# Optimization experiments

Hardware: AMD Instinct MI355X
Metric: run time of the kernel (lower is better)

The kernel has to match this reference:

```python
import jax, jax.numpy as jnp
import numpy as np

B, S, E, H = 8, 512, 1024, 16
Dh = E // H
MAX_LEN = 512


def setup_inputs() -> dict:
    key = jax.random.key(0)
    ks = jax.random.split(key, 16)
    std = 1.0 / np.sqrt(E)
    inp = {
        "query": jax.random.normal(ks[0], (B, S, E), jnp.float32),
        "key": jax.random.normal(ks[1], (B, S, E), jnp.float32),
        "value": jax.random.normal(ks[2], (B, S, E), jnp.float32),
        "Wq": jax.random.normal(ks[3], (E, E), jnp.float32) * std,
        "bq": jax.random.normal(ks[4], (E,), jnp.float32) * std,
        "Wk": jax.random.normal(ks[5], (E, E), jnp.float32) * std,
        "bk": jax.random.normal(ks[6], (E,), jnp.float32) * std,
        "Wv": jax.random.normal(ks[7], (E, E), jnp.float32) * std,
        "bv": jax.random.normal(ks[8], (E,), jnp.float32) * std,
        "Wo": jax.random.normal(ks[9], (E, E), jnp.float32) * std,
        "bo": jax.random.normal(ks[10], (E,), jnp.float32) * std,
        "pos": jax.random.normal(ks[11], (MAX_LEN, 1, E), jnp.float32),
    }
    return inp


def reference(query, key, value, Wq, bq, Wk, bk, Wv, bv, Wo, bo, pos):
    b, sq, e = query.shape
    s = min(sq, key.shape[1])  # target_seq_length (static)
    scale = np.sqrt(Dh).astype(np.float32)
    pe = pos[:s, 0, :][None]  # [1, s, E] broadcast over batch
    q = query[:, :s] @ Wq.T + bq + pe
    k = key[:, :s] @ Wk.T + bk + pe
    v = value[:, :s] @ Wv.T + bv + pe
    # [b, s, H, Dh]
    q = q.reshape(b, s, H, Dh)
    k = k.reshape(b, s, H, Dh)
    v = v.reshape(b, s, H, Dh)
    scores = jnp.einsum("bqhd,bkhd->bhqk", q, k) / scale
    attn = jax.nn.softmax(scores, axis=-1)
    wv = jnp.einsum("bhqk,bkhd->bqhd", attn, v).reshape(b, s, e)
    return wv @ Wo.T + bo
```

## Files before the change

### kernel.cpp

```cpp
#include <hip/hip_runtime.h>
#include <hip/hip_bf16.h>

typedef __attribute__((ext_vector_type(8))) short bfx8;
typedef __attribute__((ext_vector_type(4))) short bfx4;
typedef __attribute__((ext_vector_type(4))) float fx4;

static __device__ __forceinline__ short f2bf(float f) {
  union { float f; unsigned u; } v; v.f = f;
  unsigned r = v.u + 0x7fffu + ((v.u >> 16) & 1u);
  return (short)(r >> 16);
}

static __device__ __forceinline__ void gld16(const void* g, void* l) {
  __builtin_amdgcn_global_load_lds(
      (const __attribute__((address_space(1))) void*)g,
      (__attribute__((address_space(3))) void*)l, 16, 0, 0);
}

constexpr int Bz = 8, Sq = 512, Em = 1024, Hn = 16, Dh = 64;
constexpr int Mrows = Bz * Sq;
constexpr size_t NE = (size_t)Mrows * Em;
constexpr size_t WE = (size_t)Em * Em;

__global__ __launch_bounds__(256) void convert_kernel(
    const float* __restrict__ q, const float* __restrict__ k,
    const float* __restrict__ v,
    const float* __restrict__ Wq, const float* __restrict__ Wk,
    const float* __restrict__ Wv, const float* __restrict__ Wo,
    short* __restrict__ qx, short* __restrict__ kx, short* __restrict__ vx,
    short* __restrict__ wqb, short* __restrict__ wkb,
    short* __restrict__ wvb, short* __restrict__ wob)
{
  const size_t c = (size_t)blockIdx.x * 256 + threadIdx.x;
  constexpr size_t CI = NE / 8;
  constexpr size_t CW = WE / 8;
  const float* src; short* dst; size_t off;
  if (c < 3 * CI) {
    const int sgi = (int)(c / CI);
    src = sgi == 0 ? q : sgi == 1 ? k : v;
    dst = sgi == 0 ? qx : sgi == 1 ? kx : vx;
    off = (c - (size_t)sgi * CI) * 8;
  } else {
    const size_t w = c - 3 * CI;
    const int sgi = (int)(w / CW);
    src = sgi == 0 ? Wq : sgi == 1 ? Wk : sgi == 2 ? Wv : Wo;
    dst = sgi == 0 ? wqb : sgi == 1 ? wkb : sgi == 2 ? wvb : wob;
    off = (w - (size_t)sgi * CW) * 8;
  }
  fx4 a = *(const fx4*)(src + off);
  fx4 b = *(const fx4*)(src + off + 4);
  bfx8 o = { f2bf(a[0]), f2bf(a[1]), f2bf(a[2]), f2bf(a[3]),
             f2bf(b[0]), f2bf(b[1]), f2bf(b[2]), f2bf(b[3]) };
  *(bfx8*)(dst + off) = o;
}

__global__ __launch_bounds__(512, 2) void gemm_qkv_bf16(
    const short* __restrict__ qx, const short* __restrict__ kx,
    const short* __restrict__ vx,
    const short* __restrict__ Wqb, const short* __restrict__ Wkb,
    const short* __restrict__ Wvb,
    const float* __restrict__ bq, const float* __restrict__ bk,
    const float* __restrict__ bv,
    const float* __restrict__ pos,
    short* __restrict__ qb, short* __restrict__ kb, short* __restrict__ vb)
{
  __shared__ short SM[65536];

  const int z = blockIdx.z;
  const short* X = (z == 0) ? qx : (z == 1) ? kx : vx;
  const short* W = (z == 0) ? Wqb : (z == 1) ? Wkb : Wvb;
  const float* bias = (z == 0) ? bq : (z == 1) ? bk : bv;
  short* dst = (z == 0) ? qb : (z == 1) ? kb : vb;

  const int t0b = blockIdx.x * 256;
  const int f0 = blockIdx.y * 256;
  const int t = threadIdx.x, lane = t & 63, wave = t >> 6;
  const int wr = wave >> 2;
  const int wn = wave & 3;
  const int fr = lane & 15, fq = lane >> 4;

  const int srow = t >> 2;
  const int scol = ((t & 3) ^ ((t >> 3) & 3)) * 8;
  const short* gA = W + (size_t)(f0 + srow) * Em + scol;
  const short* gB = X + (size_t)(t0b + srow) * Em + scol;
  const int ldst = wave * 512;

  auto stage = [&](int ktn) {
    short* sl = SM + (ktn & 3) * 16384;
    const int ko = ktn * 32;
#pragma unroll
    for (int g = 0; g < 2; ++g) {
      gld16(gA + (size_t)(g * 128) * Em + ko, sl + g * 4096 + ldst);
      gld16(gB + (size_t)(g * 128) * Em + ko, sl + 8192 + g * 4096 + ldst);
    }
  };

  const int csw = (fq ^ ((fr >> 1) & 3)) * 8;

  fx4 acc[8][4] = {};

  stage(0); stage(1); stage(2);
  for (int kt = 0; kt < 32; ++kt) {
    if (kt < 29) stage(kt + 3);
    __builtin_amdgcn_sched_barrier(0);
    if (kt < 29)       asm volatile("s_waitcnt vmcnt(12)");
    else if (kt == 29) asm volatile("s_waitcnt vmcnt(8)");
    else if (kt == 30) asm volatile("s_waitcnt vmcnt(4)");
    else               asm volatile("s_waitcnt vmcnt(0)");
    __builtin_amdgcn_sched_barrier(0);
    __builtin_amdgcn_s_barrier();

    const short* slA = SM + (kt & 3) * 16384;
    const short* slB = slA + 8192;

    bfx8 af[8], bf[4];
#pragma unroll
    for (int rg = 0; rg < 8; ++rg)
      af[rg] = *(const bfx8*)&slA[(wr * 128 + rg * 16 + fr) * 32 + csw];
#pragma unroll
    for (int cg = 0; cg < 4; ++cg)
      bf[cg] = *(const bfx8*)&slB[(wn * 64 + cg * 16 + fr) * 32 + csw];

    __builtin_amdgcn_s_setprio(1);
#pragma unroll
    for (int rg = 0; rg < 8; ++rg)
#pragma unroll
      for (int cg = 0; cg < 4; ++cg)
        acc[rg][cg] = __builtin_amdgcn_mfma_f32_16x16x32_bf16(
            af[rg], bf[cg], acc[rg][cg], 0, 0, 0);
    __builtin_amdgcn_s_setprio(0);
    __builtin_amdgcn_sched_barrier(0);
    __builtin_amdgcn_s_barrier();
  }

  const int b = t0b >> 9;
  if (z < 2) {
#pragma unroll
    for (int fp = 0; fp < 2; ++fp) {
      if (fp) __syncthreads();
      if (wr == fp) {
#pragma unroll
        for (int rg = 0; rg < 8; ++rg) {
          const int nloc = rg * 16 + fq * 4;
          const int nng = f0 + fp * 128 + nloc;
          const fx4 bb = *(const fx4*)&bias[nng];
#pragma unroll
          for (int cg = 0; cg < 4; ++cg) {
            const int token = wn * 64 + cg * 16 + fr;
            const int s = (t0b + token) & (Sq - 1);
            const fx4 pe = *(const fx4*)&pos[(size_t)s * Em + nng];
            const fx4 a = acc[rg][cg];
            bfx4 o = { f2bf(a[0] + bb[0] + pe[0]), f2bf(a[1] + bb[1] + pe[1]),
                       f2bf(a[2] + bb[2] + pe[2]), f2bf(a[3] + bb[3] + pe[3]) };
            *(bfx4*)&SM[token * 136 + nloc] = o;
          }
        }
      }
      __syncthreads();
#pragma unroll
      for (int it = 0; it < 8; ++it) {
        const int flat = it * 512 + t;
        const int token = flat >> 4, ch = flat & 15;
        bfx8 val = *(const bfx8*)&SM[token * 136 + ch * 8];
        const int nng = f0 + fp * 128 + ch * 8;
        const int h = nng >> 6, d = nng & 63;
        const int s = (t0b + token) & (Sq - 1);
        *(bfx8*)&dst[(((size_t)b * Hn + h) * Sq + s) * Dh + d] = val;
      }
    }
  } else {
#pragma unroll
    for (int fp = 0; fp < 2; ++fp) {
      if (fp) __syncthreads();
      if (wr == fp) {
#pragma unroll
        for (int rg = 0; rg < 8; ++rg) {
          const int nloc = rg * 16 + fq * 4;
          const int nng = f0 + fp * 128 + nloc;
          const fx4 bb = *(const fx4*)&bias[nng];
#pragma unroll
          for (int cg = 0; cg < 4; ++cg) {
            const int token = wn * 64 + cg * 16 + fr;
            const int s = (t0b + token) & (Sq - 1);
            const fx4 pe = *(const fx4*)&pos[(size_t)s * Em + nng];
            const fx4 a = acc[rg][cg];
#pragma unroll
            for (int i = 0; i < 4; ++i)
              SM[(nloc + i) * 264 + token] = f2bf(a[i] + bb[i] + pe[i]);
          }
        }
      }
      __syncthreads();
      const int s0 = t0b & (Sq - 1);
#pragma unroll
      for (int it = 0; it < 8; ++it) {
        const int flat = it * 512 + t;
        const int row = flat >> 5, ch = flat & 31;
        bfx8 val = *(const bfx8*)&SM[row * 264 + ch * 8];
        const int nng = f0 + fp * 128 + row;
        const int h = nng >> 6, d = nng & 63;
        *(bfx8*)&dst[(((size_t)b * Hn + h) * Dh + d) * Sq + s0 + ch * 8] = val;
      }
    }
  }
}

constexpr int LDP = 136;

__global__ __launch_bounds__(256, 4) void gemm_out_bf16(
    const short* __restrict__ wv, const short* __restrict__ Wob,
    const float* __restrict__ bo, float* __restrict__ out)
{
  __shared__ short SMo[2 * 8192];
  short* As = SMo;
  short* Bs = SMo + 8192;

  const int m0 = blockIdx.x * 128;
  const int n0 = blockIdx.y * 128;
  const int t = threadIdx.x, lane = t & 63, wave = t >> 6;
  const int wr = wave >> 1, wc = wave & 1;
  const int fr = lane & 15, fq = lane >> 4;

  const int trow = t >> 3;
  const int scol = ((t & 7) ^ (trow & 7)) * 8;
  const short* gW = Wob + (size_t)(n0 + trow) * Em + scol;
  const short* gX = wv + (size_t)(m0 + trow) * Em + scol;
  short* lA = As + wave * 512;
  short* lB = Bs + wave * 512;

  const int sw0 = ((fq ^ (fr & 7)) * 8);
  const int sw1 = (((4 + fq) ^ (fr & 7)) * 8);

  fx4 acc[4][4] = {};

  for (int k0 = 0; k0 < Em; k0 += 64) {
#pragma unroll
    for (int r = 0; r < 4; ++r) {
      gld16(gW + (size_t)(32 * r) * Em + k0, lA + r * 2048);
      gld16(gX + (size_t)(32 * r) * Em + k0, lB + r * 2048);
    }
    __syncthreads();

#pragma unroll
    for (int ks = 0; ks < 2; ++ks) {
      const int sw = ks ? sw1 : sw0;
      bfx8 af[4], bf[4];
#pragma unroll
      for (int u = 0; u < 4; ++u)
        af[u] = *(const bfx8*)&As[(wr * 64 + u * 16 + fr) * 64 + sw];
#pragma unroll
      for (int v = 0; v < 4; ++v)
        bf[v] = *(const bfx8*)&Bs[(wc * 64 + v * 16 + fr) * 64 + sw];
#pragma unroll
      for (int u = 0; u < 4; ++u)
#pragma unroll
        for (int v = 0; v < 4; ++v)
          acc[u][v] = __builtin_amdgcn_mfma_f32_16x16x32_bf16(af[u], bf[v], acc[u][v], 0, 0, 0);
    }
    __syncthreads();
  }

#pragma unroll
  for (int u = 0; u < 4; ++u) {
    const int nn = n0 + wr * 64 + u * 16 + fq * 4;
    const fx4 bb = *(const fx4*)&bo[nn];
#pragma unroll
    for (int v = 0; v < 4; ++v) {
      const int m = m0 + wc * 64 + v * 16 + fr;
      fx4 val = acc[u][v];
      val[0] += bb[0]; val[1] += bb[1]; val[2] += bb[2]; val[3] += bb[3];
      *(fx4*)&out[(size_t)m * Em + nn] = val;
    }
  }
}

constexpr int KVB = 64, LDK = 72;

__global__ __launch_bounds__(512) void attn_kernel(
    const short* __restrict__ qb, const short* __restrict__ kb,
    const short* __restrict__ vb, short* __restrict__ wv)
{
  __shared__ short Ks[KVB * LDK];
  __shared__ short Vt[Dh * LDK];
  __shared__ short Ps[8][16 * LDK];

  const int bh = blockIdx.x;
  const int qt = blockIdx.y;
  const int t = threadIdx.x, lane = t & 63, wave = t >> 6;
  const int fr = lane & 15, fq = lane >> 4;

  const size_t base = (size_t)bh * Sq * Dh;
  const int q0 = qt * 128 + wave * 16;

  bfx8 qf[2];
  {
    const short* qp = qb + base + (size_t)(q0 + fr) * Dh;
    qf[0] = *(const bfx8*)(qp + fq * 8);
    qf[1] = *(const bfx8*)(qp + 32 + fq * 8);
  }

  const int kr = t >> 3, kc = (t & 7) * 8;
  const short* kbp = kb + base + (size_t)kr * Dh + kc;
  const short* vbp = vb + base + (size_t)kr * Sq + kc;

  {
    bfx8 k0 = *(const bfx8*)kbp;
    bfx8 v0 = *(const bfx8*)vbp;
    *(bfx8*)&Ks[kr * LDK + kc] = k0;
    *(bfx8*)&Vt[kr * LDK + kc] = v0;
  }
  __syncthreads();

  float mrow[4] = { -1e30f, -1e30f, -1e30f, -1e30f };
  float lrow[4] = { 0.f, 0.f, 0.f, 0.f };
  fx4 oacc[4] = {};

  for (int kv0 = 0; kv0 < Sq; kv0 += KVB) {
    const bool more = (kv0 + KVB) < Sq;
    bfx8 nk0, nv0;
    if (more) {
      nk0 = *(const bfx8*)(kbp + (size_t)(kv0 + KVB) * Dh);
      nv0 = *(const bfx8*)(vbp + kv0 + KVB);
    }

    fx4 sa[4] = {};
    __builtin_amdgcn_s_setprio(1);
#pragma unroll
    for (int nf = 0; nf < 4; ++nf) {
#pragma unroll
      for (int ks = 0; ks < 2; ++ks) {
        bfx8 kf = *(const bfx8*)&Ks[(nf * 16 + fr) * LDK + ks * 32 + fq * 8];
        sa[nf] = __builtin_amdgcn_mfma_f32_16x16x32_bf16(qf[ks], kf, sa[nf], 0, 0, 0);
      }
    }
    __builtin_amdgcn_s_setprio(0);

#pragma unroll
    for (int i = 0; i < 4; ++i) {
      float mx = fmaxf(fmaxf(sa[0][i], sa[1][i]), fmaxf(sa[2][i], sa[3][i]));
      mx = fmaxf(mx, __shfl_xor(mx, 1));
      mx = fmaxf(mx, __shfl_xor(mx, 2));
      mx = fmaxf(mx, __shfl_xor(mx, 4));
      mx = fmaxf(mx, __shfl_xor(mx, 8));
      mx *= 0.125f;
      if (mx > mrow[i] + 8.f) {
        const float alpha = __expf(mrow[i] - mx);
        mrow[i] = mx;
        lrow[i] *= alpha;
#pragma unroll
        for (int df = 0; df < 4; ++df) oacc[df][i] *= alpha;
      }
      float rs = 0.f;
#pragma unroll
      for (int nf = 0; nf < 4; ++nf) {
        const float p = __expf(sa[nf][i] * 0.125f - mrow[i]);
        rs += p;
        Ps[wave][(fq * 4 + i) * LDK + nf * 16 + fr] = f2bf(p);
      }
      rs += __shfl_xor(rs, 1);
      rs += __shfl_xor(rs, 2);
      rs += __shfl_xor(rs, 4);
      rs += __shfl_xor(rs, 8);
      lrow[i] += rs;
    }

    bfx8 pf[2];
    pf[0] = *(const bfx8*)&Ps[wave][fr * LDK + fq * 8];
    pf[1] = *(const bfx8*)&Ps[wave][fr * LDK + 32 + fq * 8];
    __builtin_amdgcn_s_setprio(1);
#pragma unroll
    for (int df = 0; df < 4; ++df) {
#pragma unroll
      for (int ks = 0; ks < 2; ++ks) {
        bfx8 vf = *(const bfx8*)&Vt[(df * 16 + fr) * LDK + ks * 32 + fq * 8];
        oacc[df] = __builtin_amdgcn_mfma_f32_16x16x32_bf16(pf[ks], vf, oacc[df], 0, 0, 0);
      }
    }
    __builtin_amdgcn_s_setprio(0);
    __syncthreads();

    if (more) {
      *(bfx8*)&Ks[kr * LDK + kc] = nk0;
      *(bfx8*)&Vt[kr * LDK + kc] = nv0;
      __syncthreads();
    }
  }

  const int b = bh >> 4, h = bh & 15;
#pragma unroll
  for (int df = 0; df < 4; ++df) {
    const int d = df * 16 + fr;
#pragma unroll
    for (int i = 0; i < 4; ++i) {
      const int qrow = q0 + fq * 4 + i;
      const float o = oacc[df][i] / lrow[i];
      wv[((size_t)b * Sq + qrow) * Em + h * Dh + d] = f2bf(o);
    }
  }
}

extern "C" void kernel_launch(void* const* d_in, const int* in_sizes, int n_in,
                              void* d_out, int out_size, void* d_ws, size_t ws_size,
                              hipStream_t stream) {
  (void)in_sizes; (void)n_in; (void)out_size; (void)ws_size;
  const float* query = (const float*)d_in[0];
  const float* key   = (const float*)d_in[1];
  const float* value = (const float*)d_in[2];
  const float* Wq = (const float*)d_in[3];
  const float* bq = (const float*)d_in[4];
  const float* Wk = (const float*)d_in[5];
  const float* bk = (const float*)d_in[6];
  const float* Wv = (const float*)d_in[7];
  const float* bv = (const float*)d_in[8];
  const float* Wo = (const float*)d_in[9];
  const float* bo = (const float*)d_in[10];
  const float* pos = (const float*)d_in[11];

  short* qx = (short*)d_ws;
  short* kx = qx + NE;
  short* vx = kx + NE;
  short* Wqb = vx + NE;
  short* Wkb = Wqb + WE;
  short* Wvb = Wkb + WE;
  short* Wob = Wvb + WE;
  short* qb = Wob + WE;
  short* wv = qx;
  short* kb = (short*)d_out;
  short* vb = kb + NE;

  convert_kernel<<<dim3(8192), 256, 0, stream>>>(
      query, key, value, Wq, Wk, Wv, Wo, qx, kx, vx, Wqb, Wkb, Wvb, Wob);
  gemm_qkv_bf16<<<dim3(Mrows / 256, Em / 256, 3), 512, 0, stream>>>(
      qx, kx, vx, Wqb, Wkb, Wvb, bq, bk, bv, pos, qb, kb, vb);
  attn_kernel<<<dim3(Bz * Hn, Sq / 128), 512, 0, stream>>>(qb, kb, vb, wv);
  gemm_out_bf16<<<dim3(Mrows / 128, Em / 128), 256, 0, stream>>>(
      wv, Wob, bo, (float*)d_out);
}
```

Measured before the change: 111.8 us.

## Shrink GEMM tiles and switch QKV projection to double-buffered pipeline

The QKV projection GEMM goes from a 256x256 tile with a 4-stage LDS ring to a 128x256 tile with 2-stage double buffering. Its LDS use drops to 48 KB and the occupancy hint rises to 4 blocks, and the epilogue is rewritten with an XOR swizzle on the transposed V store. The output projection GEMM tile also shrinks from 128x128 to 128x64, doubling its grid. The aim is more blocks and better latency hiding across the 256 CUs, at the cost of less data reuse per tile and a shallower prefetch pipeline.

```diff
diff --git a/kernel.cpp b/kernel.cpp
--- a/kernel.cpp
+++ b/kernel.cpp
@@ -54,7 +54,7 @@
   *(bfx8*)(dst + off) = o;
 }
 
-__global__ __launch_bounds__(512, 2) void gemm_qkv_bf16(
+__global__ __launch_bounds__(512, 4) void gemm_qkv_bf16(
     const short* __restrict__ qx, const short* __restrict__ kx,
     const short* __restrict__ vx,
     const short* __restrict__ Wqb, const short* __restrict__ Wkb,
@@ -64,7 +64,7 @@
     const float* __restrict__ pos,
     short* __restrict__ qb, short* __restrict__ kb, short* __restrict__ vb)
 {
-  __shared__ short SM[65536];
+  __shared__ short SM[24576];
 
   const int z = blockIdx.z;
   const short* X = (z == 0) ? qx : (z == 1) ? kx : vx;
@@ -73,10 +73,10 @@
   short* dst = (z == 0) ? qb : (z == 1) ? kb : vb;
 
   const int t0b = blockIdx.x * 256;
-  const int f0 = blockIdx.y * 256;
+  const int f0 = blockIdx.y * 128;
   const int t = threadIdx.x, lane = t & 63, wave = t >> 6;
-  const int wr = wave >> 2;
-  const int wn = wave & 3;
+  const int wf = wave & 1;
+  const int wt = wave >> 1;
   const int fr = lane & 15, fq = lane >> 4;
 
   const int srow = t >> 2;
@@ -85,137 +85,137 @@
   const short* gB = X + (size_t)(t0b + srow) * Em + scol;
   const int ldst = wave * 512;
 
-  auto stage = [&](int ktn) {
-    short* sl = SM + (ktn & 3) * 16384;
+  auto stage = [&](int ktn, int s) {
+    short* base = SM + s * 12288;
     const int ko = ktn * 32;
-#pragma unroll
-    for (int g = 0; g < 2; ++g) {
-      gld16(gA + (size_t)(g * 128) * Em + ko, sl + g * 4096 + ldst);
-      gld16(gB + (size_t)(g * 128) * Em + ko, sl + 8192 + g * 4096 + ldst);
-    }
+    gld16(gA + ko, base + ldst);
+    gld16(gB + ko, base + 4096 + ldst);
+    gld16(gB + (size_t)128 * Em + ko, base + 8192 + ldst);
   };
 
   const int csw = (fq ^ ((fr >> 1) & 3)) * 8;
 
-  fx4 acc[8][4] = {};
-
-  stage(0); stage(1); stage(2);
+  fx4 acc[4][4] = {};
+
+  stage(0, 0);
+  __builtin_amdgcn_sched_barrier(0);
+  asm volatile("s_waitcnt vmcnt(0)");
+  __builtin_amdgcn_sched_barrier(0);
+  __builtin_amdgcn_s_barrier();
+
   for (int kt = 0; kt < 32; ++kt) {
-    if (kt < 29) stage(kt + 3);
+    const int s = kt & 1;
+    const short* bA = SM + s * 12288;
+    const short* bB = bA + 4096;
+    const bool pre = (kt + 1 < 32);
+    if (pre) stage(kt + 1, s ^ 1);
     __builtin_amdgcn_sched_barrier(0);
-    if (kt < 29)       asm volatile("s_waitcnt vmcnt(12)");
-    else if (kt == 29) asm volatile("s_waitcnt vmcnt(8)");
-    else if (kt == 30) asm volatile("s_waitcnt vmcnt(4)");
-    else               asm volatile("s_waitcnt vmcnt(0)");
+
+    bfx8 af[4], bf[4];
+#pragma unroll
+    for (int u = 0; u < 4; ++u)
+      af[u] = *(const bfx8*)&bA[(wf * 64 + u * 16 + fr) * 32 + csw];
+#pragma unroll
+    for (int v = 0; v < 4; ++v)
+      bf[v] = *(const bfx8*)&bB[(wt * 64 + v * 16 + fr) * 32 + csw];
+
+    __builtin_amdgcn_s_setprio(1);
+#pragma unroll
+    for (int u = 0; u < 4; ++u)
+#pragma unroll
+      for (int v = 0; v < 4; ++v)
+        acc[u][v] = __builtin_amdgcn_mfma_f32_16x16x32_bf16(af[u], bf[v], acc[u][v], 0, 0, 0);
+    __builtin_amdgcn_s_setprio(0);
+    __builtin_amdgcn_sched_barrier(0);
+
+    if (pre) asm volatile("s_waitcnt vmcnt(0)");
     __builtin_amdgcn_sched_barrier(0);
     __builtin_amdgcn_s_barrier();
-
-    const short* slA = SM + (kt & 3) * 16384;
-    const short* slB = slA + 8192;
-
-    bfx8 af[8], bf[4];
-#pragma unroll
-    for (int rg = 0; rg < 8; ++rg)
-      af[rg] = *(const bfx8*)&slA[(wr * 128 + rg * 16 + fr) * 32 + csw];
-#pragma unroll
-    for (int cg = 0; cg < 4; ++cg)
-      bf[cg] = *(const bfx8*)&slB[(wn * 64 + cg * 16 + fr) * 32 + csw];
-
-    __builtin_amdgcn_s_setprio(1);
-#pragma unroll
-    for (int rg = 0; rg < 8; ++rg)
-#pragma unroll
-      for (int cg = 0; cg < 4; ++cg)
-        acc[rg][cg] = __builtin_amdgcn_mfma_f32_16x16x32_bf16(
-            af[rg], bf[cg], acc[rg][cg], 0, 0, 0);
-    __builtin_amdgcn_s_setprio(0);
-    __builtin_amdgcn_sched_barrier(0);
-    __builtin_amdgcn_s_barrier();
   }
 
   const int b = t0b >> 9;
   if (z < 2) {
 #pragma unroll
+    for (int p = 0; p < 2; ++p) {
+      if (p) __syncthreads();
+      if ((wt >> 1) == p) {
+#pragma unroll
+        for (int u = 0; u < 4; ++u) {
+          const int nloc = wf * 64 + u * 16 + fq * 4;
+          const int nng = f0 + nloc;
+          const fx4 bb = *(const fx4*)&bias[nng];
+#pragma unroll
+          for (int v = 0; v < 4; ++v) {
+            const int token = wt * 64 + v * 16 + fr;
+            const int tl = token - p * 128;
+            const int s = (t0b + token) & (Sq - 1);
+            const fx4 pe = *(const fx4*)&pos[(size_t)s * Em + nng];
+            const fx4 a = acc[u][v];
+            bfx4 o = { f2bf(a[0] + bb[0] + pe[0]), f2bf(a[1] + bb[1] + pe[1]),
+                       f2bf(a[2] + bb[2] + pe[2]), f2bf(a[3] + bb[3] + pe[3]) };
+            *(bfx4*)&SM[tl * 136 + nloc] = o;
+          }
+        }
+      }
+      __syncthreads();
+#pragma unroll
+      for (int it = 0; it < 4; ++it) {
+        const int flat = it * 512 + t;
+        const int tl = flat >> 4, ch = flat & 15;
+        bfx8 val = *(const bfx8*)&SM[tl * 136 + ch * 8];
+        const int nng = f0 + ch * 8;
+        const int h = nng >> 6, d = nng & 63;
+        const int s = (t0b + p * 128 + tl) & (Sq - 1);
+        *(bfx8*)&dst[(((size_t)b * Hn + h) * Sq + s) * Dh + d] = val;
+      }
+    }
+  } else {
+#pragma unroll
     for (int fp = 0; fp < 2; ++fp) {
       if (fp) __syncthreads();
-      if (wr == fp) {
-#pragma unroll
-        for (int rg = 0; rg < 8; ++rg) {
-          const int nloc = rg * 16 + fq * 4;
-          const int nng = f0 + fp * 128 + nloc;
+      if (wf == fp) {
+#pragma unroll
+        for (int u = 0; u < 4; ++u) {
+          const int nloc = u * 16 + fq * 4;
+          const int nng = f0 + fp * 64 + nloc;
           const fx4 bb = *(const fx4*)&bias[nng];
 #pragma unroll
-          for (int cg = 0; cg < 4; ++cg) {
-            const int token = wn * 64 + cg * 16 + fr;
+          for (int v = 0; v < 4; ++v) {
+            const int token = wt * 64 + v * 16 + fr;
             const int s = (t0b + token) & (Sq - 1);
             const fx4 pe = *(const fx4*)&pos[(size_t)s * Em + nng];
-            const fx4 a = acc[rg][cg];
-            bfx4 o = { f2bf(a[0] + bb[0] + pe[0]), f2bf(a[1] + bb[1] + pe[1]),
-                       f2bf(a[2] + bb[2] + pe[2]), f2bf(a[3] + bb[3] + pe[3]) };
-            *(bfx4*)&SM[token * 136 + nloc] = o;
+            const fx4 a = acc[u][v];
+#pragma unroll
+            for (int i = 0; i < 4; ++i) {
+              const int row = nloc + i;
+              SM[row * 264 + (token ^ ((row & 12) << 2))] = f2bf(a[i] + bb[i] + pe[i]);
+            }
           }
         }
       }
       __syncthreads();
-#pragma unroll
-      for (int it = 0; it < 8; ++it) {
-        const int flat = it * 512 + t;
-        const int token = flat >> 4, ch = flat & 15;
-        bfx8 val = *(const bfx8*)&SM[token * 136 + ch * 8];
-        const int nng = f0 + fp * 128 + ch * 8;
-        const int h = nng >> 6, d = nng & 63;
-        const int s = (t0b + token) & (Sq - 1);
-        *(bfx8*)&dst[(((size_t)b * Hn + h) * Sq + s) * Dh + d] = val;
-      }
-    }
-  } else {
-#pragma unroll
-    for (int fp = 0; fp < 2; ++fp) {
-      if (fp) __syncthreads();
-      if (wr == fp) {
-#pragma unroll
-        for (int rg = 0; rg < 8; ++rg) {
-          const int nloc = rg * 16 + fq * 4;
-          const int nng = f0 + fp * 128 + nloc;
-          const fx4 bb = *(const fx4*)&bias[nng];
-#pragma unroll
-          for (int cg = 0; cg < 4; ++cg) {
-            const int token = wn * 64 + cg * 16 + fr;
-            const int s = (t0b + token) & (Sq - 1);
-            const fx4 pe = *(const fx4*)&pos[(size_t)s * Em + nng];
-            const fx4 a = acc[rg][cg];
-#pragma unroll
-            for (int i = 0; i < 4; ++i)
-              SM[(nloc + i) * 264 + token] = f2bf(a[i] + bb[i] + pe[i]);
-          }
-        }
-      }
-      __syncthreads();
       const int s0 = t0b & (Sq - 1);
 #pragma unroll
-      for (int it = 0; it < 8; ++it) {
+      for (int it = 0; it < 4; ++it) {
         const int flat = it * 512 + t;
         const int row = flat >> 5, ch = flat & 31;
-        bfx8 val = *(const bfx8*)&SM[row * 264 + ch * 8];
-        const int nng = f0 + fp * 128 + row;
+        bfx8 val = *(const bfx8*)&SM[row * 264 + ((ch * 8) ^ ((row & 12) << 2))];
+        const int nng = f0 + fp * 64 + row;
         const int h = nng >> 6, d = nng & 63;
         *(bfx8*)&dst[(((size_t)b * Hn + h) * Dh + d) * Sq + s0 + ch * 8] = val;
       }
     }
   }
 }
-
-constexpr int LDP = 136;
 
 __global__ __launch_bounds__(256, 4) void gemm_out_bf16(
     const short* __restrict__ wv, const short* __restrict__ Wob,
     const float* __restrict__ bo, float* __restrict__ out)
 {
-  __shared__ short SMo[2 * 8192];
-  short* As = SMo;
-  short* Bs = SMo + 8192;
-
-  const int m0 = blockIdx.x * 128;
+  __shared__ short As[128 * 64];
+  __shared__ short Bs[64 * 64];
+
+  const int m0 = blockIdx.x * 64;
   const int n0 = blockIdx.y * 128;
   const int t = threadIdx.x, lane = t & 63, wave = t >> 6;
   const int wr = wave >> 1, wc = wave & 1;
@@ -225,36 +225,36 @@
   const int scol = ((t & 7) ^ (trow & 7)) * 8;
   const short* gW = Wob + (size_t)(n0 + trow) * Em + scol;
   const short* gX = wv + (size_t)(m0 + trow) * Em + scol;
-  short* lA = As + wave * 512;
-  short* lB = Bs + wave * 512;
+  const int lofs = wave * 512;
 
   const int sw0 = ((fq ^ (fr & 7)) * 8);
   const int sw1 = (((4 + fq) ^ (fr & 7)) * 8);
 
-  fx4 acc[4][4] = {};
+  fx4 acc[4][2] = {};
 
   for (int k0 = 0; k0 < Em; k0 += 64) {
 #pragma unroll
-    for (int r = 0; r < 4; ++r) {
-      gld16(gW + (size_t)(32 * r) * Em + k0, lA + r * 2048);
-      gld16(gX + (size_t)(32 * r) * Em + k0, lB + r * 2048);
-    }
+    for (int g = 0; g < 4; ++g)
+      gld16(gW + (size_t)(32 * g) * Em + k0, As + g * 2048 + lofs);
+#pragma unroll
+    for (int g = 0; g < 2; ++g)
+      gld16(gX + (size_t)(32 * g) * Em + k0, Bs + g * 2048 + lofs);
     __syncthreads();
 
 #pragma unroll
     for (int ks = 0; ks < 2; ++ks) {
       const int sw = ks ? sw1 : sw0;
-      bfx8 af[4], bf[4];
+      bfx8 af[4], bf[2];
 #pragma unroll
       for (int u = 0; u < 4; ++u)
         af[u] = *(const bfx8*)&As[(wr * 64 + u * 16 + fr) * 64 + sw];
 #pragma unroll
-      for (int v = 0; v < 4; ++v)
-        bf[v] = *(const bfx8*)&Bs[(wc * 64 + v * 16 + fr) * 64 + sw];
+      for (int v = 0; v < 2; ++v)
+        bf[v] = *(const bfx8*)&Bs[(wc * 32 + v * 16 + fr) * 64 + sw];
 #pragma unroll
       for (int u = 0; u < 4; ++u)
 #pragma unroll
-        for (int v = 0; v < 4; ++v)
+        for (int v = 0; v < 2; ++v)
           acc[u][v] = __builtin_amdgcn_mfma_f32_16x16x32_bf16(af[u], bf[v], acc[u][v], 0, 0, 0);
     }
     __syncthreads();
@@ -265,8 +265,8 @@
     const int nn = n0 + wr * 64 + u * 16 + fq * 4;
     const fx4 bb = *(const fx4*)&bo[nn];
 #pragma unroll
-    for (int v = 0; v < 4; ++v) {
-      const int m = m0 + wc * 64 + v * 16 + fr;
+    for (int v = 0; v < 2; ++v) {
+      const int m = m0 + wc * 32 + v * 16 + fr;
       fx4 val = acc[u][v];
       val[0] += bb[0]; val[1] += bb[1]; val[2] += bb[2]; val[3] += bb[3];
       *(fx4*)&out[(size_t)m * Em + nn] = val;
@@ -430,9 +430,9 @@
 
   convert_kernel<<<dim3(8192), 256, 0, stream>>>(
       query, key, value, Wq, Wk, Wv, Wo, qx, kx, vx, Wqb, Wkb, Wvb, Wob);
-  gemm_qkv_bf16<<<dim3(Mrows / 256, Em / 256, 3), 512, 0, stream>>>(
+  gemm_qkv_bf16<<<dim3(Mrows / 256, Em / 128, 3), 512, 0, stream>>>(
       qx, kx, vx, Wqb, Wkb, Wvb, bq, bk, bv, pos, qb, kb, vb);
   attn_kernel<<<dim3(Bz * Hn, Sq / 128), 512, 0, stream>>>(qb, kb, vb, wv);
-  gemm_out_bf16<<<dim3(Mrows / 128, Em / 128), 256, 0, stream>>>(
+  gemm_out_bf16<<<dim3(Mrows / 64, Em / 128), 256, 0, stream>>>(
       wv, Wob, bo, (float*)d_out);
 }
```

Measured after the change: 103.5 us (median of 4 runs). 1.08x faster.
